# Kernel tuning notes

Measured on AMD Instinct MI355X. Metric: run time of the kernel, lower is better.

The kernel has to match this reference:

```python
import jax, jax.numpy as jnp
import numpy as np

Z_DIM = 3
H = 128
N_BLOCKS = 4
N = 30000
E = 180000
T = 2


def _mlp2(x, W1, b1, W2, b2):
    return jnp.maximum(x @ W1 + b1, 0.0) @ W2 + b2


def _stats(x, eps=1e-8):
    # batch mean/std as accumulated by the running-stat Normalizer (buffers -> no grad)
    m = x.mean(0)
    v = jnp.maximum((x * x).mean(0) - m * m, 0.0)
    s = jnp.maximum(jnp.sqrt(v), eps)
    return jax.lax.stop_gradient(m), jax.lax.stop_gradient(s)


def setup_inputs() -> dict:
    key = jax.random.key(0)
    ks = jax.random.split(key, 32)

    def w(k, shape, fan_in):
        return jax.random.normal(k, shape, jnp.float32) / np.sqrt(fan_in).astype(np.float32)

    inp = {}
    inp["z"] = jax.random.normal(ks[0], (T, N, Z_DIM), jnp.float32)
    inp["z_target"] = jax.random.normal(ks[1], (N, Z_DIM), jnp.float32)
    inp["pos"] = jax.random.uniform(ks[2], (N, 2), jnp.float32)
    # encoder node MLP: z_dim -> H -> H
    inp["enc_node_W1"] = w(ks[3], (Z_DIM, H), Z_DIM)
    inp["enc_node_b1"] = jnp.zeros((H,), jnp.float32)
    inp["enc_node_W2"] = w(ks[4], (H, H), H)
    inp["enc_node_b2"] = jnp.zeros((H,), jnp.float32)
    # encoder edge MLP: edge_dim(3) -> H -> H
    inp["enc_edge_W1"] = w(ks[5], (3, H), 3)
    inp["enc_edge_b1"] = jnp.zeros((H,), jnp.float32)
    inp["enc_edge_W2"] = w(ks[6], (H, H), H)
    inp["enc_edge_b2"] = jnp.zeros((H,), jnp.float32)
    # decoder MLP: H -> H -> z_dim
    inp["dec_W1"] = w(ks[7], (H, H), H)
    inp["dec_b1"] = jnp.zeros((H,), jnp.float32)
    inp["dec_W2"] = w(ks[8], (H, Z_DIM), H)
    inp["dec_b2"] = jnp.zeros((Z_DIM,), jnp.float32)
    # GraphNetBlocks, stacked over n_blocks
    inp["blk_edge_W1"] = w(ks[9], (N_BLOCKS, 3 * H, H), 3 * H)
    inp["blk_edge_b1"] = jnp.zeros((N_BLOCKS, H), jnp.float32)
    inp["blk_edge_W2"] = w(ks[10], (N_BLOCKS, H, H), H)
    inp["blk_edge_b2"] = jnp.zeros((N_BLOCKS, H), jnp.float32)
    inp["blk_node_W1"] = w(ks[11], (N_BLOCKS, 2 * H, H), 2 * H)
    inp["blk_node_b1"] = jnp.zeros((N_BLOCKS, H), jnp.float32)
    inp["blk_node_W2"] = w(ks[12], (N_BLOCKS, H, H), H)
    inp["blk_node_b2"] = jnp.zeros((N_BLOCKS, H), jnp.float32)
    # bidirectional mesh edges (triangles_to_edges output)
    inp["senders"] = jax.random.randint(ks[13], (E,), 0, N, jnp.int64)
    inp["receivers"] = jax.random.randint(ks[14], (E,), 0, N, jnp.int64)
    return inp


def reference(z, z_target, pos,
              enc_node_W1, enc_node_b1, enc_node_W2, enc_node_b2,
              enc_edge_W1, enc_edge_b1, enc_edge_W2, enc_edge_b2,
              dec_W1, dec_b1, dec_W2, dec_b2,
              blk_edge_W1, blk_edge_b1, blk_edge_W2, blk_edge_b2,
              blk_node_W1, blk_node_b1, blk_node_W2, blk_node_b2,
              senders, receivers):
    zl = z[-1]                                   # [N, z_dim]
    n_nodes = zl.shape[0]

    # --- build_graph ---
    rel = pos[senders] - pos[receivers]          # [E, 2]
    ef_raw = jnp.concatenate([rel, jnp.linalg.norm(rel, axis=1, keepdims=True)], axis=1)  # [E, 3]
    em, es = _stats(ef_raw)
    ef = _mlp2((ef_raw - em) / es, enc_edge_W1, enc_edge_b1, enc_edge_W2, enc_edge_b2)    # [E, H]
    nm, ns = _stats(zl)
    nf = _mlp2((zl - nm) / ns, enc_node_W1, enc_node_b1, enc_node_W2, enc_node_b2)        # [N, H]

    # --- message passing blocks ---
    def block(carry, p):
        nf, ef = carry
        eW1, eb1, eW2, eb2, nW1, nb1, nW2, nb2 = p
        e_in = jnp.concatenate([ef, nf[senders], nf[receivers]], axis=1)   # [E, 3H]
        ef = _mlp2(e_in, eW1, eb1, eW2, eb2) + ef
        agg = jax.ops.segment_sum(ef, receivers, num_segments=n_nodes)    # [N, H]
        n_in = jnp.concatenate([nf, agg], axis=1)                          # [N, 2H]
        nf = _mlp2(n_in, nW1, nb1, nW2, nb2) + nf
        return (nf, ef), None

    (nf, ef), _ = jax.lax.scan(block, (nf, ef),
                               (blk_edge_W1, blk_edge_b1, blk_edge_W2, blk_edge_b2,
                                blk_node_W1, blk_node_b1, blk_node_W2, blk_node_b2))

    # --- decode + loss ---
    output = _mlp2(nf, dec_W1, dec_b1, dec_W2, dec_b2)                     # [N, z_dim]
    target = z_target - zl
    om, os = _stats(target)
    target_normalized = (target - om) / os
    loss = jnp.mean((target_normalized - output) ** 2)

    z_update = jax.lax.stop_gradient(output) * os + om                     # Normalizer.inverse(detach)
    z_pred = zl + z_update
    rmse = jnp.mean(jnp.sqrt(jnp.mean((z_pred - z_target) ** 2, axis=0)))
    return z_pred, loss, rmse
```

## Files before the change

kernel.cpp:

```cpp
#include <hip/hip_runtime.h>
#include <hip/hip_bf16.h>
#include <math.h>

#define HDIM 128
#define TPB 256

typedef __attribute__((ext_vector_type(8))) short bf16x8;
typedef __attribute__((ext_vector_type(4))) float f32x4;

static inline int ceil_div(int a, int b){ return (a + b - 1) / b; }

__device__ __forceinline__ float wave_sum(float v){
#pragma unroll
  for (int o = 32; o > 0; o >>= 1) v += __shfl_down(v, o, 64);
  return v;
}

__device__ __forceinline__ short f2bf(float f){
  __hip_bfloat16 h = __float2bfloat16(f);
  return *reinterpret_cast<short*>(&h);
}
__device__ __forceinline__ float bfb2f(short s){
  unsigned int u = ((unsigned int)(unsigned short)s) << 16;
  return __builtin_bit_cast(float, u);
}

__device__ __forceinline__ void gl_lds16(const short* g, short* l){
  __builtin_amdgcn_global_load_lds(
      (const __attribute__((address_space(1))) void*)g,
      (__attribute__((address_space(3))) void*)l, 16, 0, 0);
}

__global__ void csr_hist(const int* __restrict__ rcv, int* __restrict__ deg, int E){
  int e = blockIdx.x * blockDim.x + threadIdx.x;
  if (e < E) atomicAdd(&deg[rcv[e]], 1);
}

__global__ void csr_scan(const int* __restrict__ deg, int* __restrict__ row_start,
                         int N, int E){
  __shared__ int part[1024];
  int t = threadIdx.x;
  int chunk = (N + 1023) / 1024;
  int lo = t * chunk, hi = min(lo + chunk, N);
  int s = 0;
  for (int i = lo; i < hi; i++) s += deg[i];
  part[t] = s;
  __syncthreads();
  for (int off = 1; off < 1024; off <<= 1){
    int v = (t >= off) ? part[t - off] : 0;
    __syncthreads();
    part[t] += v;
    __syncthreads();
  }
  int base = (t == 0) ? 0 : part[t - 1];
  for (int i = lo; i < hi; i++){
    row_start[i] = base;
    base += deg[i];
  }
  if (t == 1023) row_start[N] = E;
}

__global__ void edge_prep(const float* __restrict__ pos,
                          const int* __restrict__ snd,
                          const int* __restrict__ rcv,
                          int* __restrict__ cursor,
                          int* __restrict__ psnd,
                          int* __restrict__ prcv,
                          float* __restrict__ ef_raw,
                          float* __restrict__ epart, int E){
  __shared__ float red[4][6];
  int tid = threadIdx.x, w = tid >> 6, l = tid & 63;
  int e = blockIdx.x * blockDim.x + tid;
  float s[6] = {0.f,0.f,0.f,0.f,0.f,0.f};
  if (e < E){
    int si = snd[e], ri = rcv[e];
    int p = atomicAdd(&cursor[ri], 1);
    psnd[p] = si;
    prcv[p] = ri;
    float rx = pos[2*si]   - pos[2*ri];
    float ry = pos[2*si+1] - pos[2*ri+1];
    float nm = sqrtf(rx*rx + ry*ry);
    ef_raw[3*p]   = rx;
    ef_raw[3*p+1] = ry;
    ef_raw[3*p+2] = nm;
    s[0] = rx; s[1] = ry; s[2] = nm;
    s[3] = rx*rx; s[4] = ry*ry; s[5] = nm*nm;
  }
#pragma unroll
  for (int k = 0; k < 6; k++) s[k] = wave_sum(s[k]);
  if (l == 0)
#pragma unroll
    for (int k = 0; k < 6; k++) red[w][k] = s[k];
  __syncthreads();
  if (tid < 6)
    epart[(size_t)blockIdx.x * 6 + tid] =
      red[0][tid] + red[1][tid] + red[2][tid] + red[3][tid];
}

__global__ void node_stats(const float* __restrict__ zl,
                           const float* __restrict__ z_target,
                           float* __restrict__ npart, int N){
  __shared__ float red[4][12];
  int tid = threadIdx.x, w = tid >> 6, l = tid & 63;
  int n = blockIdx.x * blockDim.x + tid;
  float s[12];
#pragma unroll
  for (int i = 0; i < 12; i++) s[i] = 0.f;
  if (n < N){
#pragma unroll
    for (int d = 0; d < 3; d++){
      float z = zl[3*n+d];
      float t = z_target[3*n+d] - z;
      s[d]   = z;  s[3+d] = z*z;
      s[6+d] = t;  s[9+d] = t*t;
    }
  }
#pragma unroll
  for (int i = 0; i < 12; i++) s[i] = wave_sum(s[i]);
  if (l == 0)
#pragma unroll
    for (int i = 0; i < 12; i++) red[w][i] = s[i];
  __syncthreads();
  if (tid < 12)
    npart[(size_t)blockIdx.x * 12 + tid] =
      red[0][tid] + red[1][tid] + red[2][tid] + red[3][tid];
}

__global__ void reduce_stats(const float* __restrict__ ep, int ne,
                             const float* __restrict__ np_, int nn,
                             float* __restrict__ raw){
  __shared__ float red[4];
  int tid = threadIdx.x, w = tid >> 6, l = tid & 63;
  for (int j = 0; j < 6; j++){
    float s = 0.f;
    for (int b = tid; b < ne; b += 256) s += ep[(size_t)b * 6 + j];
    s = wave_sum(s);
    if (l == 0) red[w] = s;
    __syncthreads();
    if (tid == 0) raw[j] = red[0] + red[1] + red[2] + red[3];
    __syncthreads();
  }
  for (int j = 0; j < 12; j++){
    float s = 0.f;
    for (int b = tid; b < nn; b += 256) s += np_[(size_t)b * 12 + j];
    s = wave_sum(s);
    if (l == 0) red[w] = s;
    __syncthreads();
    if (tid == 0) raw[6 + j] = red[0] + red[1] + red[2] + red[3];
    __syncthreads();
  }
}

__global__ void finalize_stats(const float* __restrict__ raw,
                               float* __restrict__ fin, int E, int N){
#pragma unroll
  for (int d = 0; d < 3; d++){
    float cE = (float)E, cN = (float)N;
    float m, v;
    m = raw[0+d] / cE; v = fmaxf(raw[3+d]/cE - m*m, 0.f);
    fin[0+d] = m;  fin[3+d]  = fmaxf(sqrtf(v), 1e-8f);
    m = raw[6+d] / cN; v = fmaxf(raw[9+d]/cN - m*m, 0.f);
    fin[6+d] = m;  fin[9+d]  = fmaxf(sqrtf(v), 1e-8f);
    m = raw[12+d] / cN; v = fmaxf(raw[15+d]/cN - m*m, 0.f);
    fin[12+d] = m; fin[15+d] = fmaxf(sqrtf(v), 1e-8f);
  }
}

__global__ void pack_weights(const float* __restrict__ encEW2,
                             const float* __restrict__ encNW2,
                             const float* __restrict__ decW1,
                             const float* __restrict__ beW1,
                             const float* __restrict__ beW2,
                             const float* __restrict__ bnW1,
                             const float* __restrict__ bnW2,
                             __hip_bfloat16* __restrict__ wp){
  int y = blockIdx.y;
  const float* src; __hip_bfloat16* dst; int K;
  if (y == 0){ src = encEW2; dst = wp;          K = 128; }
  else if (y == 1){ src = encNW2; dst = wp + 16384; K = 128; }
  else if (y == 2){ src = decW1;  dst = wp + 32768; K = 128; }
  else {
    int b = (y - 3) >> 2, j = (y - 3) & 3;
    __hip_bfloat16* base = wp + 49152 + b * 114688;
    if (j == 0){ src = beW1 + b*49152; dst = base;          K = 384; }
    else if (j == 1){ src = beW2 + b*16384; dst = base + 49152; K = 128; }
    else if (j == 2){ src = bnW1 + b*32768; dst = base + 65536; K = 256; }
    else { src = bnW2 + b*16384; dst = base + 98304; K = 128; }
  }
  int id = blockIdx.x * blockDim.x + threadIdx.x;
  if (id >= 128 * K) return;
  int c = id >> 12;
  int r = id & 4095;
  int t = r >> 9;
  int l = (r >> 3) & 63;
  int j = r & 7;
  int k = c * 32 + ((l >> 4) << 3) + j;
  int n = t * 16 + (l & 15);
  dst[id] = __float2bfloat16(src[k * 128 + n]);
}

__launch_bounds__(256)
__global__ void encoder_fused(const float* __restrict__ raw,
                              const float* __restrict__ mptr,
                              const float* __restrict__ sptr,
                              const float* __restrict__ W1,
                              const float* __restrict__ b1,
                              const __hip_bfloat16* __restrict__ W2f,
                              const float* __restrict__ b2,
                              __hip_bfloat16* __restrict__ out, int rows){
  __shared__ __align__(16) short bsh[16384];
  const int tid = threadIdx.x, w = tid >> 6, l = tid & 63, m = l & 15, q = l >> 4;
  const short* wsrc = (const short*)W2f;
#pragma unroll
  for (int i = 0; i < 8; i++){
    int inst = w * 8 + i;
    gl_lds16(wsrc + inst * 512 + l * 8, &bsh[inst * 512]);
  }
  float s0 = mptr[0], s1 = mptr[1], s2 = mptr[2];
  float d0 = sptr[0], d1 = sptr[1], d2 = sptr[2];
  const int row0 = blockIdx.x * 64 + w * 16;
  const int ra = min(row0 + m, rows - 1);
  float x0 = (raw[3*ra]   - s0) / d0;
  float x1 = (raw[3*ra+1] - s1) / d1;
  float x2 = (raw[3*ra+2] - s2) / d2;
  bf16x8 afr[4];
#pragma unroll
  for (int c = 0; c < 4; c++){
    int nb = c * 32 + q * 8;
#pragma unroll
    for (int j = 0; j < 8; j++){
      float h = b1[nb+j] + x0 * W1[nb+j] + x1 * W1[128+nb+j] + x2 * W1[256+nb+j];
      afr[c][j] = f2bf(fmaxf(h, 0.f));
    }
  }
  f32x4 acc[8];
#pragma unroll
  for (int t = 0; t < 8; t++) acc[t] = (f32x4){0.f,0.f,0.f,0.f};
  __syncthreads();
#pragma unroll
  for (int c = 0; c < 4; c++){
#pragma unroll
    for (int t = 0; t < 8; t++){
      bf16x8 b = *(const bf16x8*)&bsh[(c*8 + t)*512 + l*8];
      acc[t] = __builtin_amdgcn_mfma_f32_16x16x32_bf16(afr[c], b, acc[t], 0, 0, 0);
    }
  }
  const int row_d = row0 + q * 4;
#pragma unroll
  for (int t = 0; t < 8; t++){
    int col = t * 16 + m;
    float bb = b2[col];
#pragma unroll
    for (int r = 0; r < 4; r++){
      int e = row_d + r;
      if (e < rows) out[(size_t)e * HDIM + col] = __float2bfloat16(acc[t][r] + bb);
    }
  }
}

__launch_bounds__(256)
__global__ void gemm128_g(const __hip_bfloat16* __restrict__ A,
                          const __hip_bfloat16* __restrict__ Wf,
                          const float* __restrict__ bias,
                          float* __restrict__ out, int rows){
  __shared__ __align__(16) short bsh[16384];
  const int tid = threadIdx.x, w = tid >> 6, l = tid & 63, m = l & 15, q = l >> 4;
  const short* wsrc = (const short*)Wf;
#pragma unroll
  for (int i = 0; i < 8; i++){
    int inst = w * 8 + i;
    gl_lds16(wsrc + inst * 512 + l * 8, &bsh[inst * 512]);
  }
  const int row0 = blockIdx.x * 64 + w * 16;
  const int ra = min(row0 + m, rows - 1);
  const short* pa = (const short*)A + (size_t)ra * HDIM + q * 8;
  bf16x8 afr[4];
#pragma unroll
  for (int c = 0; c < 4; c++) afr[c] = *(const bf16x8*)(pa + c * 32);
  f32x4 acc[8];
#pragma unroll
  for (int t = 0; t < 8; t++) acc[t] = (f32x4){0.f,0.f,0.f,0.f};
  __syncthreads();
#pragma unroll
  for (int c = 0; c < 4; c++){
#pragma unroll
    for (int t = 0; t < 8; t++){
      bf16x8 b = *(const bf16x8*)&bsh[(c*8 + t)*512 + l*8];
      acc[t] = __builtin_amdgcn_mfma_f32_16x16x32_bf16(afr[c], b, acc[t], 0, 0, 0);
    }
  }
  const int row_d = row0 + q * 4;
#pragma unroll
  for (int t = 0; t < 8; t++){
    int col = t * 16 + m;
    float bb = bias[col];
#pragma unroll
    for (int r = 0; r < 4; r++){
      int e = row_d + r;
      if (e < rows) out[(size_t)e * HDIM + col] = fmaxf(acc[t][r] + bb, 0.f);
    }
  }
}

__launch_bounds__(512)
__global__ void edge_block(const int* __restrict__ psnd,
                           const int* __restrict__ prcv,
                           const __hip_bfloat16* __restrict__ nf,
                           __hip_bfloat16* __restrict__ ef,
                           const __hip_bfloat16* __restrict__ Wfrag,
                           const float* __restrict__ b1,
                           const float* __restrict__ b2,
                           int E){
  __shared__ __align__(16) short bsh[2][4096];
  __shared__ __align__(16) short hsh[8][16][136];
  const int tid = threadIdx.x, w = tid >> 6, l = tid & 63, m = l & 15, q = l >> 4;
  const short* wsrc = (const short*)Wfrag;
  gl_lds16(wsrc + w*512 + l*8, &bsh[0][w*512]);

  const int row0 = blockIdx.x * 128 + w * 16;
  const int ra = min(row0 + m, E - 1);
  const int si = psnd[ra], ri = prcv[ra];
  const short* pe = (const short*)ef + (size_t)ra * HDIM + q * 8;
  const short* ps = (const short*)nf + (size_t)si * HDIM + q * 8;
  const short* pr = (const short*)nf + (size_t)ri * HDIM + q * 8;
  bf16x8 afr[12];
#pragma unroll
  for (int c = 0; c < 4; c++){
    afr[c]   = *(const bf16x8*)(pe + c * 32);
    afr[4+c] = *(const bf16x8*)(ps + c * 32);
    afr[8+c] = *(const bf16x8*)(pr + c * 32);
  }
  const int orow = row0 + (l >> 2);
  const int orc = min(orow, E - 1);
  const short* pold = (const short*)ef + (size_t)orc * HDIM + (l & 3) * 32;
  bf16x8 vold[4];
#pragma unroll
  for (int k = 0; k < 4; k++) vold[k] = *(const bf16x8*)(pold + k * 8);

  f32x4 acc[8];
#pragma unroll
  for (int t = 0; t < 8; t++) acc[t] = (f32x4){0.f,0.f,0.f,0.f};
  __syncthreads();
#pragma unroll
  for (int c = 0; c < 12; c++){
    gl_lds16(wsrc + (c+1)*4096 + w*512 + l*8, &bsh[(c+1)&1][w*512]);
    const short* bb = &bsh[c & 1][0];
#pragma unroll
    for (int t = 0; t < 8; t++){
      bf16x8 b = *(const bf16x8*)(bb + t*512 + l*8);
      acc[t] = __builtin_amdgcn_mfma_f32_16x16x32_bf16(afr[c], b, acc[t], 0, 0, 0);
    }
    __syncthreads();
  }
#pragma unroll
  for (int t = 0; t < 8; t++){
    float bb = b1[t * 16 + m];
#pragma unroll
    for (int r = 0; r < 4; r++)
      hsh[w][q*4 + r][t*16 + m] = f2bf(fmaxf(acc[t][r] + bb, 0.f));
  }
  const short* ph = &hsh[w][m][0] + q * 8;
  f32x4 acc2[8];
#pragma unroll
  for (int t = 0; t < 8; t++) acc2[t] = (f32x4){0.f,0.f,0.f,0.f};
#pragma unroll
  for (int c = 12; c < 16; c++){
    if (c + 1 < 16)
      gl_lds16(wsrc + (c+1)*4096 + w*512 + l*8, &bsh[(c+1)&1][w*512]);
    bf16x8 a = *(const bf16x8*)(ph + (c - 12) * 32);
    const short* bb = &bsh[c & 1][0];
#pragma unroll
    for (int t = 0; t < 8; t++){
      bf16x8 b = *(const bf16x8*)(bb + t*512 + l*8);
      acc2[t] = __builtin_amdgcn_mfma_f32_16x16x32_bf16(a, b, acc2[t], 0, 0, 0);
    }
    if (c < 15) __syncthreads();
  }
#pragma unroll
  for (int t = 0; t < 8; t++){
    float bb = b2[t * 16 + m];
#pragma unroll
    for (int r = 0; r < 4; r++)
      hsh[w][q*4 + r][t*16 + m] = f2bf(acc2[t][r] + bb);
  }
  if (orow < E){
    const short* src = &hsh[w][l >> 2][(l & 3) * 32];
    short* dst = (short*)ef + (size_t)orow * HDIM + (l & 3) * 32;
#pragma unroll
    for (int k = 0; k < 4; k++){
      bf16x8 vnew = *(const bf16x8*)(src + k * 8);
      bf16x8 vo;
#pragma unroll
      for (int j = 0; j < 8; j++) vo[j] = f2bf(bfb2f(vnew[j]) + bfb2f(vold[k][j]));
      *(bf16x8*)(dst + k * 8) = vo;
    }
  }
}

__launch_bounds__(512)
__global__ void node_block(const int* __restrict__ row_start,
                           const __hip_bfloat16* __restrict__ ef,
                           __hip_bfloat16* __restrict__ nf,
                           const __hip_bfloat16* __restrict__ Wfrag,
                           const float* __restrict__ b1,
                           const float* __restrict__ b2,
                           int N){
  __shared__ __align__(16) short bsh[2][4096];
  __shared__ __align__(16) short hsh[8][16][136];
  const int tid = threadIdx.x, w = tid >> 6, l = tid & 63, m = l & 15, q = l >> 4;
  const short* wsrc = (const short*)Wfrag;
  gl_lds16(wsrc + w*512 + l*8, &bsh[0][w*512]);

  const int row0 = blockIdx.x * 128 + w * 16;
  const int ra = min(row0 + m, N - 1);
  const short* pn = (const short*)nf + (size_t)ra * HDIM + q * 8;
  bf16x8 afr[8];
#pragma unroll
  for (int c = 0; c < 4; c++) afr[c] = *(const bf16x8*)(pn + c * 32);
  const int orow = row0 + (l >> 2);
  const int orc = min(orow, N - 1);
  const short* pold = (const short*)nf + (size_t)orc * HDIM + (l & 3) * 32;
  bf16x8 vold[4];
#pragma unroll
  for (int k = 0; k < 4; k++) vold[k] = *(const bf16x8*)(pold + k * 8);

  float sum[4][8];
#pragma unroll
  for (int c = 0; c < 4; c++)
#pragma unroll
    for (int j = 0; j < 8; j++) sum[c][j] = 0.f;
  int s0 = row_start[ra], s1 = row_start[ra + 1];
  for (int it = s0; it < s1; it++){
    const short* pf = (const short*)ef + (size_t)it * HDIM + q * 8;
#pragma unroll
    for (int c = 0; c < 4; c++){
      bf16x8 v = *(const bf16x8*)(pf + c * 32);
#pragma unroll
      for (int j = 0; j < 8; j++) sum[c][j] += bfb2f(v[j]);
    }
  }
#pragma unroll
  for (int c = 0; c < 4; c++)
#pragma unroll
    for (int j = 0; j < 8; j++) afr[4 + c][j] = f2bf(sum[c][j]);

  f32x4 acc[8];
#pragma unroll
  for (int t = 0; t < 8; t++) acc[t] = (f32x4){0.f,0.f,0.f,0.f};
  __syncthreads();
#pragma unroll
  for (int c = 0; c < 8; c++){
    gl_lds16(wsrc + (c+1)*4096 + w*512 + l*8, &bsh[(c+1)&1][w*512]);
    const short* bb = &bsh[c & 1][0];
#pragma unroll
    for (int t = 0; t < 8; t++){
      bf16x8 b = *(const bf16x8*)(bb + t*512 + l*8);
      acc[t] = __builtin_amdgcn_mfma_f32_16x16x32_bf16(afr[c], b, acc[t], 0, 0, 0);
    }
    __syncthreads();
  }
#pragma unroll
  for (int t = 0; t < 8; t++){
    float bb = b1[t * 16 + m];
#pragma unroll
    for (int r = 0; r < 4; r++)
      hsh[w][q*4 + r][t*16 + m] = f2bf(fmaxf(acc[t][r] + bb, 0.f));
  }
  const short* ph = &hsh[w][m][0] + q * 8;
  f32x4 acc2[8];
#pragma unroll
  for (int t = 0; t < 8; t++) acc2[t] = (f32x4){0.f,0.f,0.f,0.f};
#pragma unroll
  for (int c = 8; c < 12; c++){
    if (c + 1 < 12)
      gl_lds16(wsrc + (c+1)*4096 + w*512 + l*8, &bsh[(c+1)&1][w*512]);
    bf16x8 a = *(const bf16x8*)(ph + (c - 8) * 32);
    const short* bb = &bsh[c & 1][0];
#pragma unroll
    for (int t = 0; t < 8; t++){
      bf16x8 b = *(const bf16x8*)(bb + t*512 + l*8);
      acc2[t] = __builtin_amdgcn_mfma_f32_16x16x32_bf16(a, b, acc2[t], 0, 0, 0);
    }
    if (c < 11) __syncthreads();
  }
#pragma unroll
  for (int t = 0; t < 8; t++){
    float bb = b2[t * 16 + m];
#pragma unroll
    for (int r = 0; r < 4; r++)
      hsh[w][q*4 + r][t*16 + m] = f2bf(acc2[t][r] + bb);
  }
  if (orow < N){
    const short* src = &hsh[w][l >> 2][(l & 3) * 32];
    short* dst = (short*)nf + (size_t)orow * HDIM + (l & 3) * 32;
#pragma unroll
    for (int k = 0; k < 4; k++){
      bf16x8 vnew = *(const bf16x8*)(src + k * 8);
      bf16x8 vo;
#pragma unroll
      for (int j = 0; j < 8; j++) vo[j] = f2bf(bfb2f(vnew[j]) + bfb2f(vold[k][j]));
      *(bf16x8*)(dst + k * 8) = vo;
    }
  }
}

__global__ void dec_final(const float* __restrict__ hbuf,
                          const float* __restrict__ W2,
                          const float* __restrict__ b2,
                          float* __restrict__ outd, int rows){
  __shared__ float hl[64 * 129];
  __shared__ float Wl[HDIM * 3];
  __shared__ float bl[3];
  int t = threadIdx.x;
  int node0 = blockIdx.x * 64;
  for (int i = t; i < HDIM * 3; i += 256) Wl[i] = W2[i];
  if (t < 3) bl[t] = b2[t];
#pragma unroll
  for (int i = 0; i < 32; i++){
    int lin = t + i * 256;
    int r = lin >> 7;
    int c = lin & 127;
    int node = node0 + r;
    hl[r * 129 + c] = (node < rows) ? hbuf[(size_t)node * HDIM + c] : 0.f;
  }
  __syncthreads();
  if (t < 64){
    int node = node0 + t;
    if (node < rows){
      float a0 = bl[0], a1 = bl[1], a2 = bl[2];
      for (int k = 0; k < HDIM; k++){
        float v = hl[t * 129 + k];
        a0 += v * Wl[k * 3];
        a1 += v * Wl[k * 3 + 1];
        a2 += v * Wl[k * 3 + 2];
      }
      outd[3 * node]     = a0;
      outd[3 * node + 1] = a1;
      outd[3 * node + 2] = a2;
    }
  }
}

__global__ void epilogue(const float* __restrict__ dec_out,
                         const float* __restrict__ zl,
                         const float* __restrict__ z_target,
                         const float* __restrict__ fin,
                         float* __restrict__ d_out,
                         float* __restrict__ lpart, int N){
  __shared__ float red[4][4];
  int tid = threadIdx.x, w = tid >> 6, l = tid & 63;
  int n = blockIdx.x * blockDim.x + tid;
  float s[4] = {0.f,0.f,0.f,0.f};
  if (n < N){
#pragma unroll
    for (int d = 0; d < 3; d++){
      float om = fin[12 + d], os = fin[15 + d];
      float o   = dec_out[3*n + d];
      float zld = zl[3*n + d];
      float zt  = z_target[3*n + d];
      float tgt = zt - zld;
      float tn  = (tgt - om) / os;
      float diff = tn - o;
      s[0] += diff * diff;
      float zp = zld + o * os + om;
      d_out[3*n + d] = zp;
      float e = zp - zt;
      s[1 + d] = e * e;
    }
  }
#pragma unroll
  for (int k = 0; k < 4; k++) s[k] = wave_sum(s[k]);
  if (l == 0)
#pragma unroll
    for (int k = 0; k < 4; k++) red[w][k] = s[k];
  __syncthreads();
  if (tid < 4)
    lpart[(size_t)blockIdx.x * 4 + tid] =
      red[0][tid] + red[1][tid] + red[2][tid] + red[3][tid];
}

__global__ void finalize_out(const float* __restrict__ lpart, int nb,
                             float* __restrict__ d_out, int N){
  __shared__ float red[4];
  __shared__ float vals[4];
  int tid = threadIdx.x, w = tid >> 6, l = tid & 63;
  for (int j = 0; j < 4; j++){
    float s = 0.f;
    for (int b = tid; b < nb; b += 256) s += lpart[(size_t)b * 4 + j];
    s = wave_sum(s);
    if (l == 0) red[w] = s;
    __syncthreads();
    if (tid == 0) vals[j] = red[0] + red[1] + red[2] + red[3];
    __syncthreads();
  }
  if (tid == 0){
    float cN = (float)N;
    float loss = vals[0] / (3.f * cN);
    float rmse = (sqrtf(vals[1] / cN) + sqrtf(vals[2] / cN) + sqrtf(vals[3] / cN)) / 3.f;
    d_out[(size_t)3 * N]     = loss;
    d_out[(size_t)3 * N + 1] = rmse;
  }
}

extern "C" void kernel_launch(void* const* d_in, const int* in_sizes, int n_in,
                              void* d_out, int out_size, void* d_ws, size_t ws_size,
                              hipStream_t stream){
  const float* z           = (const float*)d_in[0];
  const float* z_target    = (const float*)d_in[1];
  const float* pos         = (const float*)d_in[2];
  const float* enc_node_W1 = (const float*)d_in[3];
  const float* enc_node_b1 = (const float*)d_in[4];
  const float* enc_node_W2 = (const float*)d_in[5];
  const float* enc_node_b2 = (const float*)d_in[6];
  const float* enc_edge_W1 = (const float*)d_in[7];
  const float* enc_edge_b1 = (const float*)d_in[8];
  const float* enc_edge_W2 = (const float*)d_in[9];
  const float* enc_edge_b2 = (const float*)d_in[10];
  const float* dec_W1      = (const float*)d_in[11];
  const float* dec_b1      = (const float*)d_in[12];
  const float* dec_W2      = (const float*)d_in[13];
  const float* dec_b2      = (const float*)d_in[14];
  const float* blk_edge_W1 = (const float*)d_in[15];
  const float* blk_edge_b1 = (const float*)d_in[16];
  const float* blk_edge_W2 = (const float*)d_in[17];
  const float* blk_edge_b2 = (const float*)d_in[18];
  const float* blk_node_W1 = (const float*)d_in[19];
  const float* blk_node_b1 = (const float*)d_in[20];
  const float* blk_node_W2 = (const float*)d_in[21];
  const float* blk_node_b2 = (const float*)d_in[22];
  const int*   senders     = (const int*)d_in[23];
  const int*   receivers   = (const int*)d_in[24];

  const int N = in_sizes[1] / 3;
  const int E = in_sizes[23];
  const float* zl = z + (size_t)N * 3;

  const int neb = ceil_div(E, TPB);
  const int nnb = ceil_div(N, TPB);

  char* p = (char*)d_ws;
  auto carve = [&](size_t bytes) -> char* {
    char* r = p; p += (bytes + 255) & ~(size_t)255; return r;
  };
  float* stats_raw = (float*)carve(32 * 4);
  float* stats_fin = (float*)carve(32 * 4);
  float* epart     = (float*)carve((size_t)neb * 6 * 4);
  float* npart     = (float*)carve((size_t)nnb * 12 * 4);
  float* lpart     = (float*)carve((size_t)nnb * 4 * 4);
  float* ef_raw    = (float*)carve((size_t)E * 3 * 4);
  float* dec_out   = (float*)carve((size_t)N * 3 * 4);
  float* hbuf      = (float*)carve((size_t)N * HDIM * 4);
  int*   deg       = (int*)carve((size_t)N * 4);
  int*   row_start = (int*)carve((size_t)(N + 1) * 4);
  int*   cursor    = (int*)carve((size_t)N * 4);
  int*   psnd      = (int*)carve((size_t)E * 4);
  int*   prcv      = (int*)carve((size_t)E * 4);
  __hip_bfloat16* wp = (__hip_bfloat16*)carve((size_t)507904 * 2);
  __hip_bfloat16* ef = (__hip_bfloat16*)carve((size_t)E * HDIM * 2);
  __hip_bfloat16* nf = (__hip_bfloat16*)carve((size_t)N * HDIM * 2);

  float* out = (float*)d_out;

  hipMemsetAsync(deg, 0, (size_t)N * 4, stream);

  csr_hist<<<neb, TPB, 0, stream>>>(receivers, deg, E);
  csr_scan<<<1, 1024, 0, stream>>>(deg, row_start, N, E);
  hipMemcpyAsync(cursor, row_start, (size_t)N * 4, hipMemcpyDeviceToDevice, stream);
  edge_prep<<<neb, TPB, 0, stream>>>(pos, senders, receivers, cursor,
                                     psnd, prcv, ef_raw, epart, E);

  node_stats<<<nnb, TPB, 0, stream>>>(zl, z_target, npart, N);
  reduce_stats<<<1, TPB, 0, stream>>>(epart, neb, npart, nnb, stats_raw);
  finalize_stats<<<1, 1, 0, stream>>>(stats_raw, stats_fin, E, N);

  pack_weights<<<dim3(192, 19), TPB, 0, stream>>>(enc_edge_W2, enc_node_W2, dec_W1,
                                                  blk_edge_W1, blk_edge_W2,
                                                  blk_node_W1, blk_node_W2, wp);

  encoder_fused<<<ceil_div(E, 64), TPB, 0, stream>>>(ef_raw, stats_fin + 0, stats_fin + 3,
                                                     enc_edge_W1, enc_edge_b1,
                                                     wp, enc_edge_b2, ef, E);
  encoder_fused<<<ceil_div(N, 64), TPB, 0, stream>>>(zl, stats_fin + 6, stats_fin + 9,
                                                     enc_node_W1, enc_node_b1,
                                                     wp + 16384, enc_node_b2, nf, N);

  for (int b = 0; b < 4; b++){
    const __hip_bfloat16* eWf = wp + 49152 + (size_t)b * 114688;
    const __hip_bfloat16* nWf = eWf + 65536;
    const float* eb1 = blk_edge_b1 + (size_t)b * 128;
    const float* eb2 = blk_edge_b2 + (size_t)b * 128;
    const float* nb1 = blk_node_b1 + (size_t)b * 128;
    const float* nb2 = blk_node_b2 + (size_t)b * 128;

    edge_block<<<ceil_div(E, 128), 512, 0, stream>>>(psnd, prcv, nf, ef,
                                                     eWf, eb1, eb2, E);
    node_block<<<ceil_div(N, 128), 512, 0, stream>>>(row_start, ef, nf,
                                                     nWf, nb1, nb2, N);
  }

  gemm128_g<<<ceil_div(N, 64), TPB, 0, stream>>>(nf, wp + 32768, dec_b1, hbuf, N);
  dec_final<<<ceil_div(N, 64), TPB, 0, stream>>>(hbuf, dec_W2, dec_b2, dec_out, N);

  epilogue<<<nnb, TPB, 0, stream>>>(dec_out, zl, z_target, stats_fin,
                                    out, lpart, N);
  finalize_out<<<1, TPB, 0, stream>>>(lpart, nnb, out, N);
}
```

Before: 561.5 us.

## Keep full edge MLP weights in LDS and loop over multiple row tiles per block

The edge block kernel now loads the entire 128 KB weight fragment set into LDS once per block. It then processes 768 edges per block with 4 waves, each wave doing 6 passes of two 16-row tiles. The per-chunk weight streaming and its barriers are gone, and the next pass's gathered sender, receiver and edge fragments are prefetched during the current pass. The trade-off is very high LDS use, so only one block fits per CU, only about 235 blocks are launched, and register pressure rises, all of which reduce occupancy and latency hiding.

```diff
diff --git a/kernel.cpp b/kernel.cpp
--- a/kernel.cpp
+++ b/kernel.cpp
@@ -4,6 +4,8 @@
 
 #define HDIM 128
 #define TPB 256
+#define EPASS 6
+#define EROWS_BLK 768
 
 typedef __attribute__((ext_vector_type(8))) short bf16x8;
 typedef __attribute__((ext_vector_type(4))) float f32x4;
@@ -302,7 +304,7 @@
   }
 }
 
-__launch_bounds__(512)
+__launch_bounds__(256)
 __global__ void edge_block(const int* __restrict__ psnd,
                            const int* __restrict__ prcv,
                            const __hip_bfloat16* __restrict__ nf,
@@ -311,89 +313,104 @@
                            const float* __restrict__ b1,
                            const float* __restrict__ b2,
                            int E){
-  __shared__ __align__(16) short bsh[2][4096];
-  __shared__ __align__(16) short hsh[8][16][136];
+  __shared__ __align__(16) short wsh[65536];
+  __shared__ __align__(16) short hsh[4][16][136];
   const int tid = threadIdx.x, w = tid >> 6, l = tid & 63, m = l & 15, q = l >> 4;
   const short* wsrc = (const short*)Wfrag;
-  gl_lds16(wsrc + w*512 + l*8, &bsh[0][w*512]);
-
-  const int row0 = blockIdx.x * 128 + w * 16;
-  const int ra = min(row0 + m, E - 1);
-  const int si = psnd[ra], ri = prcv[ra];
-  const short* pe = (const short*)ef + (size_t)ra * HDIM + q * 8;
-  const short* ps = (const short*)nf + (size_t)si * HDIM + q * 8;
-  const short* pr = (const short*)nf + (size_t)ri * HDIM + q * 8;
-  bf16x8 afr[12];
-#pragma unroll
-  for (int c = 0; c < 4; c++){
-    afr[c]   = *(const bf16x8*)(pe + c * 32);
-    afr[4+c] = *(const bf16x8*)(ps + c * 32);
-    afr[8+c] = *(const bf16x8*)(pr + c * 32);
-  }
-  const int orow = row0 + (l >> 2);
-  const int orc = min(orow, E - 1);
-  const short* pold = (const short*)ef + (size_t)orc * HDIM + (l & 3) * 32;
-  bf16x8 vold[4];
-#pragma unroll
-  for (int k = 0; k < 4; k++) vold[k] = *(const bf16x8*)(pold + k * 8);
-
-  f32x4 acc[8];
-#pragma unroll
-  for (int t = 0; t < 8; t++) acc[t] = (f32x4){0.f,0.f,0.f,0.f};
-  __syncthreads();
-#pragma unroll
-  for (int c = 0; c < 12; c++){
-    gl_lds16(wsrc + (c+1)*4096 + w*512 + l*8, &bsh[(c+1)&1][w*512]);
-    const short* bb = &bsh[c & 1][0];
-#pragma unroll
-    for (int t = 0; t < 8; t++){
-      bf16x8 b = *(const bf16x8*)(bb + t*512 + l*8);
-      acc[t] = __builtin_amdgcn_mfma_f32_16x16x32_bf16(afr[c], b, acc[t], 0, 0, 0);
-    }
-    __syncthreads();
-  }
-#pragma unroll
-  for (int t = 0; t < 8; t++){
-    float bb = b1[t * 16 + m];
-#pragma unroll
-    for (int r = 0; r < 4; r++)
-      hsh[w][q*4 + r][t*16 + m] = f2bf(fmaxf(acc[t][r] + bb, 0.f));
-  }
-  const short* ph = &hsh[w][m][0] + q * 8;
-  f32x4 acc2[8];
-#pragma unroll
-  for (int t = 0; t < 8; t++) acc2[t] = (f32x4){0.f,0.f,0.f,0.f};
-#pragma unroll
-  for (int c = 12; c < 16; c++){
-    if (c + 1 < 16)
-      gl_lds16(wsrc + (c+1)*4096 + w*512 + l*8, &bsh[(c+1)&1][w*512]);
-    bf16x8 a = *(const bf16x8*)(ph + (c - 12) * 32);
-    const short* bb = &bsh[c & 1][0];
-#pragma unroll
-    for (int t = 0; t < 8; t++){
-      bf16x8 b = *(const bf16x8*)(bb + t*512 + l*8);
-      acc2[t] = __builtin_amdgcn_mfma_f32_16x16x32_bf16(a, b, acc2[t], 0, 0, 0);
-    }
-    if (c < 15) __syncthreads();
-  }
-#pragma unroll
-  for (int t = 0; t < 8; t++){
-    float bb = b2[t * 16 + m];
-#pragma unroll
-    for (int r = 0; r < 4; r++)
-      hsh[w][q*4 + r][t*16 + m] = f2bf(acc2[t][r] + bb);
-  }
-  if (orow < E){
-    const short* src = &hsh[w][l >> 2][(l & 3) * 32];
-    short* dst = (short*)ef + (size_t)orow * HDIM + (l & 3) * 32;
-#pragma unroll
-    for (int k = 0; k < 4; k++){
-      bf16x8 vnew = *(const bf16x8*)(src + k * 8);
-      bf16x8 vo;
-#pragma unroll
-      for (int j = 0; j < 8; j++) vo[j] = f2bf(bfb2f(vnew[j]) + bfb2f(vold[k][j]));
-      *(bf16x8*)(dst + k * 8) = vo;
-    }
+#pragma unroll
+  for (int i = 0; i < 32; i++){
+    int inst = w * 32 + i;
+    gl_lds16(wsrc + inst * 512 + l * 8, &wsh[inst * 512]);
+  }
+
+  const int wbase = blockIdx.x * EROWS_BLK + w * (EPASS * 32);
+  float vb1[8], vb2[8];
+#pragma unroll
+  for (int t = 0; t < 8; t++){ vb1[t] = b1[t*16 + m]; vb2[t] = b2[t*16 + m]; }
+
+  auto loadA = [&](int row0, bf16x8* A){
+    int ra = min(row0 + m, E - 1);
+    int si = psnd[ra], ri = prcv[ra];
+    const short* pe = (const short*)ef + (size_t)ra * HDIM + q * 8;
+    const short* ps = (const short*)nf + (size_t)si * HDIM + q * 8;
+    const short* pr = (const short*)nf + (size_t)ri * HDIM + q * 8;
+#pragma unroll
+    for (int c = 0; c < 4; c++){
+      A[c]   = *(const bf16x8*)(pe + c * 32);
+      A[4+c] = *(const bf16x8*)(ps + c * 32);
+      A[8+c] = *(const bf16x8*)(pr + c * 32);
+    }
+  };
+
+  bf16x8 afr0[12], afr1[12];
+  loadA(wbase, afr0);
+  loadA(wbase + 16, afr1);
+  __syncthreads();
+
+#pragma unroll 1
+  for (int p = 0; p < EPASS; p++){
+    const int row0 = wbase + p * 32;
+    f32x4 acc0[8], acc1[8];
+#pragma unroll
+    for (int t = 0; t < 8; t++){ acc0[t] = (f32x4){0,0,0,0}; acc1[t] = (f32x4){0,0,0,0}; }
+#pragma unroll
+    for (int c = 0; c < 12; c++){
+#pragma unroll
+      for (int t = 0; t < 8; t++){
+        bf16x8 b = *(const bf16x8*)&wsh[((c*8 + t)*64 + l)*8];
+        acc0[t] = __builtin_amdgcn_mfma_f32_16x16x32_bf16(afr0[c], b, acc0[t], 0, 0, 0);
+        acc1[t] = __builtin_amdgcn_mfma_f32_16x16x32_bf16(afr1[c], b, acc1[t], 0, 0, 0);
+      }
+    }
+    bf16x8 nafr0[12], nafr1[12];
+    {
+      int nrow = wbase + min(p + 1, EPASS - 1) * 32;
+      loadA(nrow, nafr0);
+      loadA(nrow + 16, nafr1);
+    }
+#pragma unroll
+    for (int tile = 0; tile < 2; tile++){
+      f32x4* acc = tile ? acc1 : acc0;
+#pragma unroll
+      for (int t = 0; t < 8; t++)
+#pragma unroll
+        for (int r = 0; r < 4; r++)
+          hsh[w][q*4 + r][t*16 + m] = f2bf(fmaxf(acc[t][r] + vb1[t], 0.f));
+      const short* ph = &hsh[w][m][0] + q * 8;
+      f32x4 acc2[8];
+#pragma unroll
+      for (int t = 0; t < 8; t++) acc2[t] = (f32x4){0,0,0,0};
+#pragma unroll
+      for (int c = 0; c < 4; c++){
+        bf16x8 a = *(const bf16x8*)(ph + c * 32);
+#pragma unroll
+        for (int t = 0; t < 8; t++){
+          bf16x8 b = *(const bf16x8*)&wsh[49152 + ((c*8 + t)*64 + l)*8];
+          acc2[t] = __builtin_amdgcn_mfma_f32_16x16x32_bf16(a, b, acc2[t], 0, 0, 0);
+        }
+      }
+#pragma unroll
+      for (int t = 0; t < 8; t++)
+#pragma unroll
+        for (int r = 0; r < 4; r++)
+          hsh[w][q*4 + r][t*16 + m] = f2bf(acc2[t][r] + vb2[t]);
+      int orow = row0 + tile * 16 + (l >> 2);
+      if (orow < E){
+        const short* src = &hsh[w][l >> 2][(l & 3) * 32];
+        short* dst = (short*)ef + (size_t)orow * HDIM + (l & 3) * 32;
+#pragma unroll
+        for (int k = 0; k < 4; k++){
+          bf16x8 vnew = *(const bf16x8*)(src + k * 8);
+          bf16x8 vold = *(const bf16x8*)(dst + k * 8);
+          bf16x8 vo;
+#pragma unroll
+          for (int j = 0; j < 8; j++) vo[j] = f2bf(bfb2f(vnew[j]) + bfb2f(vold[j]));
+          *(bf16x8*)(dst + k * 8) = vo;
+        }
+      }
+    }
+#pragma unroll
+    for (int c = 0; c < 12; c++){ afr0[c] = nafr0[c]; afr1[c] = nafr1[c]; }
   }
 }
 
@@ -692,8 +709,8 @@
     const float* nb1 = blk_node_b1 + (size_t)b * 128;
     const float* nb2 = blk_node_b2 + (size_t)b * 128;
 
-    edge_block<<<ceil_div(E, 128), 512, 0, stream>>>(psnd, prcv, nf, ef,
-                                                     eWf, eb1, eb2, E);
+    edge_block<<<ceil_div(E, EROWS_BLK), TPB, 0, stream>>>(psnd, prcv, nf, ef,
+                                                           eWf, eb1, eb2, E);
     node_block<<<ceil_div(N, 128), 512, 0, stream>>>(row_start, ef, nf,
                                                      nWf, nb1, nb2, N);
   }
```

Result: slower. 574.7 us (+2.3%).

## Process two 16-row edge tiles per wave and read second-layer weights from global

Applied to the files above, without the earlier changes.

The edge_block kernel now has each wave handle 32 edges (two 16-row MFMA tiles) instead of 16, so every LDS-staged weight fragment feeds twice as many MFMAs and the grid is halved. The second-layer weights are loaded directly from global/L2 per lane instead of being double-buffered through LDS, which removes four barriers per block. In exchange, register pressure roughly doubles (24 A fragments, 16 accumulators, 8 saved residual vectors), which can lower occupancy or cause spills, and there are fewer blocks to spread across the CUs.

```diff
diff --git a/kernel.cpp b/kernel.cpp
--- a/kernel.cpp
+++ b/kernel.cpp
@@ -317,82 +317,103 @@
   const short* wsrc = (const short*)Wfrag;
   gl_lds16(wsrc + w*512 + l*8, &bsh[0][w*512]);
 
-  const int row0 = blockIdx.x * 128 + w * 16;
-  const int ra = min(row0 + m, E - 1);
-  const int si = psnd[ra], ri = prcv[ra];
-  const short* pe = (const short*)ef + (size_t)ra * HDIM + q * 8;
-  const short* ps = (const short*)nf + (size_t)si * HDIM + q * 8;
-  const short* pr = (const short*)nf + (size_t)ri * HDIM + q * 8;
-  bf16x8 afr[12];
-#pragma unroll
-  for (int c = 0; c < 4; c++){
-    afr[c]   = *(const bf16x8*)(pe + c * 32);
-    afr[4+c] = *(const bf16x8*)(ps + c * 32);
-    afr[8+c] = *(const bf16x8*)(pr + c * 32);
-  }
-  const int orow = row0 + (l >> 2);
-  const int orc = min(orow, E - 1);
-  const short* pold = (const short*)ef + (size_t)orc * HDIM + (l & 3) * 32;
-  bf16x8 vold[4];
-#pragma unroll
-  for (int k = 0; k < 4; k++) vold[k] = *(const bf16x8*)(pold + k * 8);
-
-  f32x4 acc[8];
-#pragma unroll
-  for (int t = 0; t < 8; t++) acc[t] = (f32x4){0.f,0.f,0.f,0.f};
+  const int row0 = blockIdx.x * 256 + w * 32;
+  const int ra0 = min(row0 + m, E - 1);
+  const int ra1 = min(row0 + 16 + m, E - 1);
+  const int s0i = psnd[ra0], r0i = prcv[ra0];
+  const int s1i = psnd[ra1], r1i = prcv[ra1];
+  bf16x8 afr0[12], afr1[12];
+  {
+    const short* pe0 = (const short*)ef + (size_t)ra0 * HDIM + q * 8;
+    const short* ps0 = (const short*)nf + (size_t)s0i * HDIM + q * 8;
+    const short* pr0 = (const short*)nf + (size_t)r0i * HDIM + q * 8;
+    const short* pe1 = (const short*)ef + (size_t)ra1 * HDIM + q * 8;
+    const short* ps1 = (const short*)nf + (size_t)s1i * HDIM + q * 8;
+    const short* pr1 = (const short*)nf + (size_t)r1i * HDIM + q * 8;
+#pragma unroll
+    for (int c = 0; c < 4; c++){
+      afr0[c]   = *(const bf16x8*)(pe0 + c * 32);
+      afr0[4+c] = *(const bf16x8*)(ps0 + c * 32);
+      afr0[8+c] = *(const bf16x8*)(pr0 + c * 32);
+      afr1[c]   = *(const bf16x8*)(pe1 + c * 32);
+      afr1[4+c] = *(const bf16x8*)(ps1 + c * 32);
+      afr1[8+c] = *(const bf16x8*)(pr1 + c * 32);
+    }
+  }
+  const int orow0 = row0 + (l >> 2);
+  const int orow1 = row0 + 16 + (l >> 2);
+  bf16x8 vold0[4], vold1[4];
+  {
+    const short* po0 = (const short*)ef + (size_t)min(orow0, E-1) * HDIM + (l & 3) * 32;
+    const short* po1 = (const short*)ef + (size_t)min(orow1, E-1) * HDIM + (l & 3) * 32;
+#pragma unroll
+    for (int k = 0; k < 4; k++){
+      vold0[k] = *(const bf16x8*)(po0 + k * 8);
+      vold1[k] = *(const bf16x8*)(po1 + k * 8);
+    }
+  }
+
+  f32x4 acc0[8], acc1[8];
+#pragma unroll
+  for (int t = 0; t < 8; t++){ acc0[t] = (f32x4){0,0,0,0}; acc1[t] = (f32x4){0,0,0,0}; }
   __syncthreads();
 #pragma unroll
   for (int c = 0; c < 12; c++){
-    gl_lds16(wsrc + (c+1)*4096 + w*512 + l*8, &bsh[(c+1)&1][w*512]);
+    if (c + 1 < 12)
+      gl_lds16(wsrc + (c+1)*4096 + w*512 + l*8, &bsh[(c+1)&1][w*512]);
     const short* bb = &bsh[c & 1][0];
 #pragma unroll
     for (int t = 0; t < 8; t++){
       bf16x8 b = *(const bf16x8*)(bb + t*512 + l*8);
-      acc[t] = __builtin_amdgcn_mfma_f32_16x16x32_bf16(afr[c], b, acc[t], 0, 0, 0);
-    }
-    __syncthreads();
-  }
-#pragma unroll
-  for (int t = 0; t < 8; t++){
-    float bb = b1[t * 16 + m];
-#pragma unroll
-    for (int r = 0; r < 4; r++)
-      hsh[w][q*4 + r][t*16 + m] = f2bf(fmaxf(acc[t][r] + bb, 0.f));
-  }
-  const short* ph = &hsh[w][m][0] + q * 8;
-  f32x4 acc2[8];
-#pragma unroll
-  for (int t = 0; t < 8; t++) acc2[t] = (f32x4){0.f,0.f,0.f,0.f};
-#pragma unroll
-  for (int c = 12; c < 16; c++){
-    if (c + 1 < 16)
-      gl_lds16(wsrc + (c+1)*4096 + w*512 + l*8, &bsh[(c+1)&1][w*512]);
-    bf16x8 a = *(const bf16x8*)(ph + (c - 12) * 32);
-    const short* bb = &bsh[c & 1][0];
+      acc0[t] = __builtin_amdgcn_mfma_f32_16x16x32_bf16(afr0[c], b, acc0[t], 0, 0, 0);
+      acc1[t] = __builtin_amdgcn_mfma_f32_16x16x32_bf16(afr1[c], b, acc1[t], 0, 0, 0);
+    }
+    if (c + 1 < 12) __syncthreads();
+  }
+  const short* w2 = wsrc + 49152;
+#pragma unroll
+  for (int tile = 0; tile < 2; tile++){
+    const f32x4* acc = tile ? acc1 : acc0;
+    const bf16x8* vold = tile ? vold1 : vold0;
+    const int orow = tile ? orow1 : orow0;
 #pragma unroll
     for (int t = 0; t < 8; t++){
-      bf16x8 b = *(const bf16x8*)(bb + t*512 + l*8);
-      acc2[t] = __builtin_amdgcn_mfma_f32_16x16x32_bf16(a, b, acc2[t], 0, 0, 0);
-    }
-    if (c < 15) __syncthreads();
-  }
-#pragma unroll
-  for (int t = 0; t < 8; t++){
-    float bb = b2[t * 16 + m];
-#pragma unroll
-    for (int r = 0; r < 4; r++)
-      hsh[w][q*4 + r][t*16 + m] = f2bf(acc2[t][r] + bb);
-  }
-  if (orow < E){
-    const short* src = &hsh[w][l >> 2][(l & 3) * 32];
-    short* dst = (short*)ef + (size_t)orow * HDIM + (l & 3) * 32;
-#pragma unroll
-    for (int k = 0; k < 4; k++){
-      bf16x8 vnew = *(const bf16x8*)(src + k * 8);
-      bf16x8 vo;
-#pragma unroll
-      for (int j = 0; j < 8; j++) vo[j] = f2bf(bfb2f(vnew[j]) + bfb2f(vold[k][j]));
-      *(bf16x8*)(dst + k * 8) = vo;
+      float bb = b1[t * 16 + m];
+#pragma unroll
+      for (int r = 0; r < 4; r++)
+        hsh[w][q*4 + r][t*16 + m] = f2bf(fmaxf(acc[t][r] + bb, 0.f));
+    }
+    const short* ph = &hsh[w][m][0] + q * 8;
+    f32x4 acc2[8];
+#pragma unroll
+    for (int t = 0; t < 8; t++) acc2[t] = (f32x4){0,0,0,0};
+#pragma unroll
+    for (int c = 0; c < 4; c++){
+      bf16x8 a = *(const bf16x8*)(ph + c * 32);
+#pragma unroll
+      for (int t = 0; t < 8; t++){
+        bf16x8 b = *(const bf16x8*)(w2 + ((c*8 + t)*64 + l)*8);
+        acc2[t] = __builtin_amdgcn_mfma_f32_16x16x32_bf16(a, b, acc2[t], 0, 0, 0);
+      }
+    }
+#pragma unroll
+    for (int t = 0; t < 8; t++){
+      float bb = b2[t * 16 + m];
+#pragma unroll
+      for (int r = 0; r < 4; r++)
+        hsh[w][q*4 + r][t*16 + m] = f2bf(acc2[t][r] + bb);
+    }
+    if (orow < E){
+      const short* src = &hsh[w][l >> 2][(l & 3) * 32];
+      short* dst = (short*)ef + (size_t)orow * HDIM + (l & 3) * 32;
+#pragma unroll
+      for (int k = 0; k < 4; k++){
+        bf16x8 vnew = *(const bf16x8*)(src + k * 8);
+        bf16x8 vo;
+#pragma unroll
+        for (int j = 0; j < 8; j++) vo[j] = f2bf(bfb2f(vnew[j]) + bfb2f(vold[k][j]));
+        *(bf16x8*)(dst + k * 8) = vo;
+      }
     }
   }
 }
@@ -692,7 +713,7 @@
     const float* nb1 = blk_node_b1 + (size_t)b * 128;
     const float* nb2 = blk_node_b2 + (size_t)b * 128;
 
-    edge_block<<<ceil_div(E, 128), 512, 0, stream>>>(psnd, prcv, nf, ef,
+    edge_block<<<ceil_div(E, 256), 512, 0, stream>>>(psnd, prcv, nf, ef,
                                                      eWf, eb1, eb2, E);
     node_block<<<ceil_div(N, 128), 512, 0, stream>>>(row_start, ef, nf,
                                                      nWf, nb1, nb2, N);
```

New measurement: 626.7 us. 11.6% more time.
